# Optimization experiments

Hardware: AMD Instinct MI355X
Metric: run time of the kernel (lower is better)

Reference implementation:

```python
import jax, jax.numpy as jnp
import numpy as np

EMBED_DIMS = [8, 16, 8]      # prod = 1024 = embed_dim
HIDDEN_DIMS = [16, 16, 16]   # prod = 4096 = hidden_dim
RANK = 16
B, S = 4, 1024


def _make_cores(key, in_dims, out_dims, rank):
    d = len(in_dims)
    ranks = [1] + [rank] * (d - 1) + [1]
    cores = []
    for k in range(d):
        key, sub = jax.random.split(key)
        shape = (ranks[k], in_dims[k], out_dims[k], ranks[k + 1])
        scale = 1.0 / np.sqrt(in_dims[k] * ranks[k])
        cores.append((scale * jax.random.normal(sub, shape, dtype=jnp.float32)))
    return cores


def setup_inputs() -> dict:
    key = jax.random.key(0)
    k_x, k1, k2, kb1, kb2 = jax.random.split(key, 5)
    x = jax.random.normal(k_x, (B, S, 1024), dtype=jnp.float32)
    fc1 = _make_cores(k1, EMBED_DIMS, HIDDEN_DIMS, RANK)
    fc2 = _make_cores(k2, HIDDEN_DIMS, EMBED_DIMS, RANK)
    b1 = 0.01 * jax.random.normal(kb1, (4096,), dtype=jnp.float32)
    b2 = 0.01 * jax.random.normal(kb2, (1024,), dtype=jnp.float32)
    return {
        "x": x,
        "fc1_c0": fc1[0], "fc1_c1": fc1[1], "fc1_c2": fc1[2], "fc1_b": b1,
        "fc2_c0": fc2[0], "fc2_c1": fc2[1], "fc2_c2": fc2[2], "fc2_b": b2,
    }


def tt_linear(x_flat, cores, bias, in_dims):
    """TT-matrix x batch-of-vectors product. x_flat: [N, prod(in_dims)].

    Cores: core_k has shape [r_{k-1}, n_k, m_k, r_k] with r_0 = r_d = 1.
    Invariant: acc is [r_{k-1}, n_k, rest] with rest laid out as
    (n_{k+1}..n_d, N, m_1..m_{k-1}).
    """
    N = x_flat.shape[0]
    acc = x_flat.reshape((N,) + tuple(in_dims))      # [N, n1..nd]
    acc = jnp.moveaxis(acc, 0, -1)                   # [n1..nd, N]
    acc = acc.reshape(in_dims[0], -1)[None]          # [1, n1, rest]
    d = len(cores)
    for k, c in enumerate(cores):
        # contract previous rank + current input mode
        acc = jnp.einsum('pnR,pnmq->Rmq', acc, c)    # [rest, m_k, r_k]
        if k < d - 1:
            n_next = in_dims[k + 1]
            R, m, q = acc.shape
            acc = acc.reshape(n_next, R // n_next, m, q)
            acc = jnp.transpose(acc, (3, 0, 1, 2)).reshape(q, n_next, -1)
    # final acc: [N * m1..m_{d-1}, m_d, 1] -> [N, M]
    return acc.reshape(N, -1) + bias


def reference(x, fc1_c0, fc1_c1, fc1_c2, fc1_b, fc2_c0, fc2_c1, fc2_c2, fc2_b):
    flat = x.reshape(-1, x.shape[-1])                        # [N, embed_dim]
    z1 = tt_linear(flat, [fc1_c0, fc1_c1, fc1_c2], fc1_b, EMBED_DIMS)   # [N, hidden]
    h1 = jax.nn.gelu(z1, approximate=False)                  # exact erf GELU (torch default)
    z2 = tt_linear(h1, [fc2_c0, fc2_c1, fc2_c2], fc2_b, HIDDEN_DIMS)    # [N, embed]
    return z2.reshape(*x.shape[:-1], z2.shape[-1])
```

## Files before the change

### kernel.cpp

```cpp
#include <hip/hip_runtime.h>
#include <stdint.h>

__device__ __forceinline__ float b2f(unsigned short u) {
    union { uint32_t i; float f; } v; v.i = ((uint32_t)u) << 16; return v.f;
}
__device__ __forceinline__ unsigned short f2b(float f) {
    union { float f; uint32_t i; } v; v.f = f;
    uint32_t r = v.i + 0x7fffu + ((v.i >> 16) & 1u);
    return (unsigned short)(r >> 16);
}

typedef __bf16 bf16x8 __attribute__((ext_vector_type(8)));
typedef float  f32x16 __attribute__((ext_vector_type(16)));

__global__ __launch_bounds__(256)
void cvt_f32_bf16(const float* __restrict__ x, unsigned short* __restrict__ xb) {
    int t = blockIdx.x * 256 + threadIdx.x;
    const float4* p = (const float4*)(x + (size_t)t * 8);
    float4 f0 = p[0], f1 = p[1];
    int4 o;
    o.x = (uint32_t)f2b(f0.x) | ((uint32_t)f2b(f0.y) << 16);
    o.y = (uint32_t)f2b(f0.z) | ((uint32_t)f2b(f0.w) << 16);
    o.z = (uint32_t)f2b(f1.x) | ((uint32_t)f2b(f1.y) << 16);
    o.w = (uint32_t)f2b(f1.z) | ((uint32_t)f2b(f1.w) << 16);
    ((int4*)xb)[t] = o;
}

template<int N3, int M3>
__global__ void build_T(const float* __restrict__ c1,
                        const float* __restrict__ c2,
                        float* __restrict__ T) {
    int e = blockIdx.x * 256 + threadIdx.x;
    int m3 = e % M3;
    int t  = e / M3;
    int n3 = t % N3;
    int rm = t / N3;
    float s = 0.f;
#pragma unroll
    for (int r2 = 0; r2 < 16; ++r2)
        s += c1[rm * 16 + r2] * c2[(r2 * N3 + n3) * M3 + m3];
    T[e] = s;
}

template<int N1, int N2, int N3, int M1, int M2, int M3>
__global__ __launch_bounds__(256)
void build_W(const float* __restrict__ c0,
             const float* __restrict__ T,
             unsigned short* __restrict__ W) {
    constexpr int K = N1 * N2 * N3;
    int t  = blockIdx.x * 256 + threadIdx.x;
    int m3 = t % M3;
    int m2 = (t / M3) % M2;
    int n2 = (t / (M3 * M2)) % N2;
    int m1 = (t / (M3 * M2 * N2)) % M1;
    int n1 =  t / (M3 * M2 * N2 * M1);

    float c0r[16];
    const float4* c0p = (const float4*)(c0 + (n1 * M1 + m1) * 16);
#pragma unroll
    for (int i = 0; i < 4; ++i) ((float4*)c0r)[i] = c0p[i];

    float acc[N3] = {};
#pragma unroll
    for (int r1 = 0; r1 < 16; ++r1) {
        const float* Tp = T + (size_t)(((r1 * 16 + n2) * 16 + m2) * N3) * M3 + m3;
#pragma unroll
        for (int n3 = 0; n3 < N3; ++n3)
            acc[n3] += c0r[r1] * Tp[n3 * M3];
    }

    unsigned short ob[N3];
#pragma unroll
    for (int n3 = 0; n3 < N3; ++n3) ob[n3] = f2b(acc[n3]);

    unsigned short* dst = W + (size_t)((m1 * M2 + m2) * M3 + m3) * K
                            + (n1 * N2 + n2) * N3;
#pragma unroll
    for (int c = 0; c < N3 / 8; ++c)
        ((int4*)dst)[c] = ((const int4*)ob)[c];
}

template<int BM, int BN>
__device__ __forceinline__ void stage_chunk16(
    const unsigned short* __restrict__ A,
    const unsigned short* __restrict__ Bt,
    char* __restrict__ dstbuf, int ktot,
    int rowBase, int colBase, int tk, int c, int tid)
{
    const int off  = (c * 512 + tid) * 16;
    const bool isB = off >= BM * 128;
    const int off2 = isB ? off - BM * 128 : off;
    const int r    = off2 >> 7;
    const int jg   = ((off2 >> 4) & 7) ^ (r & 7);
    const unsigned short* src = (isB ? Bt + (size_t)(colBase + r) * ktot
                                     : A  + (size_t)(rowBase + r) * ktot)
                                + tk * 64 + jg * 8;
    void* dst = dstbuf + (c * 8192 + (tid >> 6) * 1024);
    __builtin_amdgcn_global_load_lds(
        (const __attribute__((address_space(1))) void*)src,
        (__attribute__((address_space(3))) void*)dst, 16, 0, 0);
}

template<int BM, int BN, int KTOT, int NCOLS, int PPT, bool DO_GELU, bool C_F32>
__global__ __launch_bounds__(512, 2)
void gemm3p(const unsigned short* __restrict__ A,
            const unsigned short* __restrict__ Bt,
            const float* __restrict__ bias,
            void* __restrict__ Cv)
{
    constexpr int BK   = 64;
    constexpr int NT   = KTOT / BK;
    constexpr int BUFB = (BM + BN) * 128;
    constexpr int LPT  = (BM + BN) * BK * 2 / (512 * 16);
    constexpr int SPP  = LPT / PPT;
    constexpr int KPP  = 4 / PPT;
    constexpr int WGM  = 4, WGN = 2;
    constexpr int FI   = BM / (WGM * 32);
    constexpr int FJ   = BN / (WGN * 32);
    constexpr int GX   = NCOLS / BN;

    extern __shared__ char smem[];

    const int tid  = threadIdx.x;
    const int lane = tid & 63;
    const int wave = tid >> 6;
    const int m32  = lane & 31;
    const int kh   = lane >> 5;
    const int wm   = wave >> 1;
    const int wn   = wave & 1;

    int lin = blockIdx.y * GX + blockIdx.x;
    const int cpx = (int)(GX * gridDim.y) >> 3;
    lin = (lin & 7) * cpx + (lin >> 3);
    const int rowBase = (lin / GX) * BM;
    const int colBase = (lin % GX) * BN;

    f32x16 acc[FI][FJ] = {};

#pragma unroll
    for (int c = 0; c < LPT; ++c)
        stage_chunk16<BM, BN>(A, Bt, smem, KTOT, rowBase, colBase, 0, c, tid);
#pragma unroll
    for (int c = 0; c < LPT; ++c)
        stage_chunk16<BM, BN>(A, Bt, smem + BUFB, KTOT, rowBase, colBase, 1, c, tid);
    asm volatile("s_waitcnt vmcnt(%0)" :: "n"(LPT) : "memory");
    __builtin_amdgcn_s_barrier();
    asm volatile("" ::: "memory");

    int bt = 0;
    for (int t = 0; t < NT; ++t) {
        const int sb = bt >= 1 ? bt - 1 : 2;
        const char* Ab = smem + bt * BUFB;
        const char* Bb = Ab + BM * 128;
        char* Sb = smem + sb * BUFB;
        const bool doStage = (t + 2 < NT);

#pragma unroll
        for (int ph = 0; ph < PPT; ++ph) {
            bf16x8 af[FI][KPP], bfr[FJ][KPP];
#pragma unroll
            for (int i = 0; i < FI; ++i) {
                const int rr = wm * (BM / WGM) + i * 32 + m32;
#pragma unroll
                for (int u = 0; u < KPP; ++u) {
                    const int lc = (ph * KPP + u) * 2 + kh;
                    af[i][u] = *(const bf16x8*)(Ab + rr * 128 + ((lc ^ (rr & 7)) << 4));
                }
            }
#pragma unroll
            for (int j = 0; j < FJ; ++j) {
                const int rr = wn * (BN / WGN) + j * 32 + m32;
#pragma unroll
                for (int u = 0; u < KPP; ++u) {
                    const int lc = (ph * KPP + u) * 2 + kh;
                    bfr[j][u] = *(const bf16x8*)(Bb + rr * 128 + ((lc ^ (rr & 7)) << 4));
                }
            }
            if (doStage) {
#pragma unroll
                for (int c = 0; c < SPP; ++c)
                    stage_chunk16<BM, BN>(A, Bt, Sb, KTOT, rowBase, colBase,
                                          t + 2, ph * SPP + c, tid);
            }
            __builtin_amdgcn_s_barrier();
            asm volatile("s_waitcnt lgkmcnt(0)" ::: "memory");
            __builtin_amdgcn_s_setprio(1);
#pragma unroll
            for (int u = 0; u < KPP; ++u)
#pragma unroll
                for (int i = 0; i < FI; ++i)
#pragma unroll
                    for (int j = 0; j < FJ; ++j)
                        acc[i][j] = __builtin_amdgcn_mfma_f32_32x32x16_bf16(
                            af[i][u], bfr[j][u], acc[i][j], 0, 0, 0);
            __builtin_amdgcn_s_setprio(0);
            if (ph == PPT - 1) {
                if (t + 2 < NT) {
                    asm volatile("s_waitcnt vmcnt(%0)" :: "n"(LPT) : "memory");
                } else if (t + 1 < NT) {
                    asm volatile("s_waitcnt vmcnt(0)" ::: "memory");
                }
            }
            __builtin_amdgcn_s_barrier();
            asm volatile("" ::: "memory");
        }
        bt = bt < 2 ? bt + 1 : 0;
    }

    const int waveM = wm * (BM / WGM);
    const int waveN = wn * (BN / WGN);
#pragma unroll
    for (int i = 0; i < FI; ++i) {
#pragma unroll
        for (int j = 0; j < FJ; ++j) {
            const int col = colBase + waveN + j * 32 + m32;
            const float bv = bias[col];
#pragma unroll
            for (int reg = 0; reg < 16; ++reg) {
                const int row = rowBase + waveM + i * 32 +
                                (reg & 3) + 8 * (reg >> 2) + 4 * kh;
                float z = acc[i][j][reg] + bv;
                if (DO_GELU)
                    z = 0.5f * z * (1.f + erff(z * 0.70710678118654752f));
                const size_t off = (size_t)row * NCOLS + col;
                if (C_F32) ((float*)Cv)[off] = z;
                else       ((unsigned short*)Cv)[off] = f2b(z);
            }
        }
    }
}

#define PC_COMPUTE(BUF)                                                       \
    {                                                                         \
        _Pragma("unroll")                                                     \
        for (int ks = 0; ks < 4; ++ks) {                                      \
            bf16x8 a_f[FI], b_f[FJ];                                          \
            _Pragma("unroll")                                                 \
            for (int i = 0; i < FI; ++i) {                                    \
                const int key = (m32 & 7) ^                                   \
                    (((waveM >> 3) + 4 * i + (m32 >> 3)) & 7);                \
                const int slot = ((ks * 2 + khalf) ^ key) * 8;                \
                a_f[i] = *(const bf16x8*)&As[(BUF) * ASZ +                    \
                          (waveM + i * 32 + m32) * BK + slot];                \
            }                                                                 \
            _Pragma("unroll")                                                 \
            for (int j = 0; j < FJ; ++j) {                                    \
                const int key = (m32 & 7) ^                                   \
                    (((waveN >> 3) + 4 * j + (m32 >> 3)) & 7);                \
                const int slot = ((ks * 2 + khalf) ^ key) * 8;                \
                b_f[j] = *(const bf16x8*)&Bs[(BUF) * BSZ +                    \
                          (waveN + j * 32 + m32) * BK + slot];                \
            }                                                                 \
            _Pragma("unroll")                                                 \
            for (int i = 0; i < FI; ++i)                                      \
                _Pragma("unroll")                                             \
                for (int j = 0; j < FJ; ++j)                                  \
                    acc[i][j] = __builtin_amdgcn_mfma_f32_32x32x16_bf16(      \
                        a_f[i], b_f[j], acc[i][j], 0, 0, 0);                  \
        }                                                                     \
    }

template<int BM, int BN, int KTOT, bool DO_GELU, bool A_F32, bool C_F32>
__global__ __launch_bounds__(512, 4)
void gemm_pc(const void* __restrict__ Av,
             const unsigned short* __restrict__ Bt,
             const float* __restrict__ bias,
             void* __restrict__ Cv,
             int Ncols) {
    constexpr int BK  = 64;
    constexpr int CA  = BM / 8;
    constexpr int CB  = BN / 8;
    constexpr int PA  = CA / 4;
    constexpr int PB  = CB / 4;
    constexpr int FI  = BM / 64;
    constexpr int FJ  = BN / 64;
    constexpr int ASZ = BM * BK;
    constexpr int BSZ = BN * BK;
    __shared__ unsigned short As[2 * ASZ];
    __shared__ unsigned short Bs[2 * BSZ];

    const int tid  = threadIdx.x;
    const int lane = tid & 63;
    const int wave = tid >> 6;
    const int rowBase = blockIdx.y * BM;
    const int colBase = blockIdx.x * BN;

    const int lr    = lane >> 3;
    const int jj    = lane & 7;
    const int m32   = lane & 31;
    const int khalf = lane >> 5;

    if (wave >= 4) {
        const int pw = wave - 4;
#pragma unroll
        for (int it = 0; it < PA; ++it) {
            const int c  = pw * PA + it;
            const int jg = jj ^ lr ^ (c & 7);
            const size_t aoff = (size_t)(rowBase + c * 8 + lr) * KTOT + jg * 8;
            int4 v;
            if (A_F32) {
                const float* ga = (const float*)Av + aoff;
                float4 f0 = *(const float4*)ga;
                float4 f1 = *(const float4*)(ga + 4);
                v.x = (uint32_t)f2b(f0.x) | ((uint32_t)f2b(f0.y) << 16);
                v.y = (uint32_t)f2b(f0.z) | ((uint32_t)f2b(f0.w) << 16);
                v.z = (uint32_t)f2b(f1.x) | ((uint32_t)f2b(f1.y) << 16);
                v.w = (uint32_t)f2b(f1.z) | ((uint32_t)f2b(f1.w) << 16);
            } else {
                v = *(const int4*)((const unsigned short*)Av + aoff);
            }
            *(int4*)&As[c * 512 + lane * 8] = v;
        }
#pragma unroll
        for (int it = 0; it < PB; ++it) {
            const int c  = pw * PB + it;
            const int jg = jj ^ lr ^ (c & 7);
            *(int4*)&Bs[c * 512 + lane * 8] =
                *(const int4*)(Bt + (size_t)(colBase + c * 8 + lr) * KTOT + jg * 8);
        }
        __syncthreads();

        int buf = 1;
        for (int k0 = BK; k0 < KTOT; k0 += BK) {
            int4 aR[PA], bR[PB];
#pragma unroll
            for (int it = 0; it < PA; ++it) {
                const int c  = pw * PA + it;
                const int jg = jj ^ lr ^ (c & 7);
                const size_t aoff = (size_t)(rowBase + c * 8 + lr) * KTOT + k0 + jg * 8;
                if (A_F32) {
                    const float* ga = (const float*)Av + aoff;
                    float4 f0 = *(const float4*)ga;
                    float4 f1 = *(const float4*)(ga + 4);
                    int4 v;
                    v.x = (uint32_t)f2b(f0.x) | ((uint32_t)f2b(f0.y) << 16);
                    v.y = (uint32_t)f2b(f0.z) | ((uint32_t)f2b(f0.w) << 16);
                    v.z = (uint32_t)f2b(f1.x) | ((uint32_t)f2b(f1.y) << 16);
                    v.w = (uint32_t)f2b(f1.z) | ((uint32_t)f2b(f1.w) << 16);
                    aR[it] = v;
                } else {
                    aR[it] = *(const int4*)((const unsigned short*)Av + aoff);
                }
            }
#pragma unroll
            for (int it = 0; it < PB; ++it) {
                const int c  = pw * PB + it;
                const int jg = jj ^ lr ^ (c & 7);
                bR[it] = *(const int4*)(Bt + (size_t)(colBase + c * 8 + lr) * KTOT + k0 + jg * 8);
            }
#pragma unroll
            for (int it = 0; it < PA; ++it) {
                const int c = pw * PA + it;
                *(int4*)&As[buf * ASZ + c * 512 + lane * 8] = aR[it];
            }
#pragma unroll
            for (int it = 0; it < PB; ++it) {
                const int c = pw * PB + it;
                *(int4*)&Bs[buf * BSZ + c * 512 + lane * 8] = bR[it];
            }
            __syncthreads();
            buf ^= 1;
        }
    } else {
        const int waveM = (wave >> 1) * (BM / 2);
        const int waveN = (wave & 1) * (BN / 2);
        f32x16 acc[FI][FJ] = {};

        __syncthreads();

        int cur = 0;
        for (int k0 = BK; k0 < KTOT; k0 += BK) {
            PC_COMPUTE(cur)
            __syncthreads();
            cur ^= 1;
        }
        PC_COMPUTE(cur)

#pragma unroll
        for (int i = 0; i < FI; ++i) {
#pragma unroll
            for (int j = 0; j < FJ; ++j) {
                const int col = colBase + waveN + j * 32 + m32;
                const float bv = bias[col];
#pragma unroll
                for (int reg = 0; reg < 16; ++reg) {
                    const int row = rowBase + waveM + i * 32 +
                                    (reg & 3) + 8 * (reg >> 2) + 4 * khalf;
                    float z = acc[i][j][reg] + bv;
                    if (DO_GELU)
                        z = 0.5f * z * (1.f + erff(z * 0.70710678118654752f));
                    const size_t off = (size_t)row * Ncols + col;
                    if (C_F32) ((float*)Cv)[off] = z;
                    else       ((unsigned short*)Cv)[off] = f2b(z);
                }
            }
        }
    }
}

extern "C" void kernel_launch(void* const* d_in, const int* in_sizes, int n_in,
                              void* d_out, int out_size, void* d_ws, size_t ws_size,
                              hipStream_t stream) {
    const float* x      = (const float*)d_in[0];
    const float* fc1_c0 = (const float*)d_in[1];
    const float* fc1_c1 = (const float*)d_in[2];
    const float* fc1_c2 = (const float*)d_in[3];
    const float* fc1_b  = (const float*)d_in[4];
    const float* fc2_c0 = (const float*)d_in[5];
    const float* fc2_c1 = (const float*)d_in[6];
    const float* fc2_c2 = (const float*)d_in[7];
    const float* fc2_b  = (const float*)d_in[8];

    char* ws = (char*)d_ws;
    unsigned short* W  = (unsigned short*)(ws);
    float*          T  = (float*)(ws + (8u << 20));
    const bool big = ws_size >= (50ull << 20);
    unsigned short* xb = (unsigned short*)(ws + (10u << 20));
    unsigned short* h  = (unsigned short*)(ws + (big ? (18u << 20) : (10u << 20)));

    static bool attr_done = false;
    if (!attr_done) {
        attr_done = true;
        (void)hipFuncSetAttribute(
            reinterpret_cast<const void*>(&gemm3p<256, 128, 1024, 4096, 2, true, false>),
            hipFuncAttributeMaxDynamicSharedMemorySize, 3 * (256 + 128) * 128);
        (void)hipFuncSetAttribute(
            reinterpret_cast<const void*>(&gemm3p<128, 128, 4096, 1024, 1, false, true>),
            hipFuncAttributeMaxDynamicSharedMemorySize, 3 * (128 + 128) * 128);
    }

    build_T<8, 16><<<2048, 256, 0, stream>>>(fc1_c1, fc1_c2, T);
    build_W<8, 16, 8, 16, 16, 16><<<2048, 256, 0, stream>>>(fc1_c0, T, W);
    if (big) {
        cvt_f32_bf16<<<2048, 256, 0, stream>>>(x, xb);
        gemm3p<256, 128, 1024, 4096, 2, true, false>
            <<<dim3(32, 16), 512, 3 * (256 + 128) * 128, stream>>>(xb, W, fc1_b, h);
    } else {
        gemm_pc<128, 128, 1024, true, true, false>
            <<<dim3(32, 32), 512, 0, stream>>>(x, W, fc1_b, h, 4096);
    }

    build_T<16, 8><<<2048, 256, 0, stream>>>(fc2_c1, fc2_c2, T);
    build_W<16, 16, 16, 8, 16, 8><<<1024, 256, 0, stream>>>(fc2_c0, T, W);
    gemm3p<128, 128, 4096, 1024, 1, false, true>
        <<<dim3(8, 32), 512, 3 * (128 + 128) * 128, stream>>>(h, W, fc2_b, d_out);
}
```

Measured before the change: 237.5 us.

## Use 256x256 tiles with 4-stage BK=32 pipeline and split-K atomics for fc2

Replaces the GEMM kernel with a 256x256 tile variant that uses BK=32, a 4-deep LDS ring buffer and a new swizzle with precomputed per-fragment offsets. The second GEMM becomes split-K over 4 chunks: the output is pre-filled with bias and partial sums are accumulated with atomic float adds. This aims to raise arithmetic intensity per tile and fill more CUs in the fc2 GEMM, which previously had only 256 blocks. In exchange it adds atomic traffic, an extra bias-fill pass, and non-deterministic summation order.

Result: slower. 259.4 us (+9.2%).

```diff
diff --git a/kernel.cpp b/kernel.cpp
--- a/kernel.cpp
+++ b/kernel.cpp
@@ -24,6 +24,12 @@
     o.z = (uint32_t)f2b(f1.x) | ((uint32_t)f2b(f1.y) << 16);
     o.w = (uint32_t)f2b(f1.z) | ((uint32_t)f2b(f1.w) << 16);
     ((int4*)xb)[t] = o;
+}
+
+__global__ __launch_bounds__(256)
+void bias_fill(const float* __restrict__ b, float4* __restrict__ out) {
+    int t = blockIdx.x * 256 + threadIdx.x;
+    out[t] = ((const float4*)b)[t & 255];
 }
 
 template<int N3, int M3>
@@ -81,43 +87,44 @@
 }
 
 template<int BM, int BN>
-__device__ __forceinline__ void stage_chunk16(
-    const unsigned short* __restrict__ A,
-    const unsigned short* __restrict__ Bt,
-    char* __restrict__ dstbuf, int ktot,
-    int rowBase, int colBase, int tk, int c, int tid)
+__device__ __forceinline__ void stage4(const unsigned short* __restrict__ A,
+                                       const unsigned short* __restrict__ Bt,
+                                       char* __restrict__ dstbuf, int kstride,
+                                       int rowBase, int colBase, int kElem,
+                                       int c, int tid)
 {
     const int off  = (c * 512 + tid) * 16;
-    const bool isB = off >= BM * 128;
-    const int off2 = isB ? off - BM * 128 : off;
-    const int r    = off2 >> 7;
-    const int jg   = ((off2 >> 4) & 7) ^ (r & 7);
-    const unsigned short* src = (isB ? Bt + (size_t)(colBase + r) * ktot
-                                     : A  + (size_t)(rowBase + r) * ktot)
-                                + tk * 64 + jg * 8;
+    const bool isB = off >= BM * 64;
+    const int off2 = isB ? off - BM * 64 : off;
+    const int r    = off2 >> 6;
+    const int slot = (off2 >> 4) & 3;
+    const int key  = ((r >> 1) ^ (r >> 3)) & 3;
+    const int g    = slot ^ key;
+    const unsigned short* src = (isB ? Bt + (size_t)(colBase + r) * kstride
+                                     : A  + (size_t)(rowBase + r) * kstride)
+                                + kElem + g * 8;
     void* dst = dstbuf + (c * 8192 + (tid >> 6) * 1024);
     __builtin_amdgcn_global_load_lds(
         (const __attribute__((address_space(1))) void*)src,
         (__attribute__((address_space(3))) void*)dst, 16, 0, 0);
 }
 
-template<int BM, int BN, int KTOT, int NCOLS, int PPT, bool DO_GELU, bool C_F32>
+template<int BM, int BN, int KCH, int NCOLS, int GX, int GY,
+         bool DO_GELU, bool ATOMIC>
 __global__ __launch_bounds__(512, 2)
-void gemm3p(const unsigned short* __restrict__ A,
+void gemm4r(const unsigned short* __restrict__ A,
             const unsigned short* __restrict__ Bt,
             const float* __restrict__ bias,
-            void* __restrict__ Cv)
+            void* __restrict__ Cv,
+            int kstride)
 {
-    constexpr int BK   = 64;
-    constexpr int NT   = KTOT / BK;
-    constexpr int BUFB = (BM + BN) * 128;
+    constexpr int BK   = 32;
+    constexpr int NT   = KCH / BK;
+    constexpr int BUFB = (BM + BN) * 64;
     constexpr int LPT  = (BM + BN) * BK * 2 / (512 * 16);
-    constexpr int SPP  = LPT / PPT;
-    constexpr int KPP  = 4 / PPT;
-    constexpr int WGM  = 4, WGN = 2;
-    constexpr int FI   = BM / (WGM * 32);
-    constexpr int FJ   = BN / (WGN * 32);
-    constexpr int GX   = NCOLS / BN;
+    constexpr int WGM = 2, WGN = 4;
+    constexpr int FI = BM / (WGM * 32);
+    constexpr int FJ = BN / (WGN * 32);
 
     extern __shared__ char smem[];
 
@@ -126,85 +133,89 @@
     const int wave = tid >> 6;
     const int m32  = lane & 31;
     const int kh   = lane >> 5;
-    const int wm   = wave >> 1;
-    const int wn   = wave & 1;
-
-    int lin = blockIdx.y * GX + blockIdx.x;
-    const int cpx = (int)(GX * gridDim.y) >> 3;
+    const int wm   = wave >> 2;
+    const int wn   = wave & 3;
+
+    int lin = ((int)blockIdx.z * GY + (int)blockIdx.y) * GX + (int)blockIdx.x;
+    const int total = GX * GY * (int)gridDim.z;
+    const int cpx = total >> 3;
     lin = (lin & 7) * cpx + (lin >> 3);
-    const int rowBase = (lin / GX) * BM;
-    const int colBase = (lin % GX) * BN;
+    const int colT = lin % GX;
+    const int rowT = (lin / GX) % GY;
+    const int kz   = lin / (GX * GY);
+    const int rowBase = rowT * BM;
+    const int colBase = colT * BN;
+    const int kOff    = kz * KCH;
+
+    int aOff[FI], aKey[FI];
+#pragma unroll
+    for (int i = 0; i < FI; ++i) {
+        const int r = wm * (BM / WGM) + i * 32 + m32;
+        aOff[i] = r * 64;
+        aKey[i] = ((r >> 1) ^ (r >> 3)) & 3;
+    }
+    int bOff[FJ], bKey[FJ];
+#pragma unroll
+    for (int j = 0; j < FJ; ++j) {
+        const int r = wn * (BN / WGN) + j * 32 + m32;
+        bOff[j] = BM * 64 + r * 64;
+        bKey[j] = ((r >> 1) ^ (r >> 3)) & 3;
+    }
 
     f32x16 acc[FI][FJ] = {};
 
 #pragma unroll
-    for (int c = 0; c < LPT; ++c)
-        stage_chunk16<BM, BN>(A, Bt, smem, KTOT, rowBase, colBase, 0, c, tid);
-#pragma unroll
-    for (int c = 0; c < LPT; ++c)
-        stage_chunk16<BM, BN>(A, Bt, smem + BUFB, KTOT, rowBase, colBase, 1, c, tid);
-    asm volatile("s_waitcnt vmcnt(%0)" :: "n"(LPT) : "memory");
+    for (int tt = 0; tt < 3; ++tt)
+#pragma unroll
+        for (int c = 0; c < LPT; ++c)
+            stage4<BM, BN>(A, Bt, smem + tt * BUFB, kstride,
+                           rowBase, colBase, kOff + tt * BK, c, tid);
+    asm volatile("s_waitcnt vmcnt(8)" ::: "memory");
     __builtin_amdgcn_s_barrier();
     asm volatile("" ::: "memory");
 
-    int bt = 0;
     for (int t = 0; t < NT; ++t) {
-        const int sb = bt >= 1 ? bt - 1 : 2;
-        const char* Ab = smem + bt * BUFB;
-        const char* Bb = Ab + BM * 128;
-        char* Sb = smem + sb * BUFB;
-        const bool doStage = (t + 2 < NT);
-
-#pragma unroll
-        for (int ph = 0; ph < PPT; ++ph) {
-            bf16x8 af[FI][KPP], bfr[FJ][KPP];
-#pragma unroll
-            for (int i = 0; i < FI; ++i) {
-                const int rr = wm * (BM / WGM) + i * 32 + m32;
-#pragma unroll
-                for (int u = 0; u < KPP; ++u) {
-                    const int lc = (ph * KPP + u) * 2 + kh;
-                    af[i][u] = *(const bf16x8*)(Ab + rr * 128 + ((lc ^ (rr & 7)) << 4));
-                }
-            }
-#pragma unroll
-            for (int j = 0; j < FJ; ++j) {
-                const int rr = wn * (BN / WGN) + j * 32 + m32;
-#pragma unroll
-                for (int u = 0; u < KPP; ++u) {
-                    const int lc = (ph * KPP + u) * 2 + kh;
-                    bfr[j][u] = *(const bf16x8*)(Bb + rr * 128 + ((lc ^ (rr & 7)) << 4));
-                }
-            }
-            if (doStage) {
-#pragma unroll
-                for (int c = 0; c < SPP; ++c)
-                    stage_chunk16<BM, BN>(A, Bt, Sb, KTOT, rowBase, colBase,
-                                          t + 2, ph * SPP + c, tid);
-            }
-            __builtin_amdgcn_s_barrier();
-            asm volatile("s_waitcnt lgkmcnt(0)" ::: "memory");
-            __builtin_amdgcn_s_setprio(1);
-#pragma unroll
-            for (int u = 0; u < KPP; ++u)
-#pragma unroll
-                for (int i = 0; i < FI; ++i)
-#pragma unroll
-                    for (int j = 0; j < FJ; ++j)
-                        acc[i][j] = __builtin_amdgcn_mfma_f32_32x32x16_bf16(
-                            af[i][u], bfr[j][u], acc[i][j], 0, 0, 0);
-            __builtin_amdgcn_s_setprio(0);
-            if (ph == PPT - 1) {
-                if (t + 2 < NT) {
-                    asm volatile("s_waitcnt vmcnt(%0)" :: "n"(LPT) : "memory");
-                } else if (t + 1 < NT) {
-                    asm volatile("s_waitcnt vmcnt(0)" ::: "memory");
-                }
-            }
+        char* base = smem + (t & 3) * BUFB;
+
+        if (t + 3 < NT) {
+            char* sb = smem + ((t + 3) & 3) * BUFB;
+#pragma unroll
+            for (int c = 0; c < LPT; ++c)
+                stage4<BM, BN>(A, Bt, sb, kstride, rowBase, colBase,
+                               kOff + (t + 3) * BK, c, tid);
+        }
+
+        __builtin_amdgcn_s_setprio(1);
+#pragma unroll
+        for (int u = 0; u < 2; ++u) {
+            bf16x8 af[FI], bfr[FJ];
+            const int lc = u * 2 + kh;
+#pragma unroll
+            for (int i = 0; i < FI; ++i)
+                af[i] = *(const bf16x8*)(base + aOff[i] + ((lc ^ aKey[i]) << 4));
+#pragma unroll
+            for (int j = 0; j < FJ; ++j)
+                bfr[j] = *(const bf16x8*)(base + bOff[j] + ((lc ^ bKey[j]) << 4));
+#pragma unroll
+            for (int i = 0; i < FI; ++i)
+#pragma unroll
+                for (int j = 0; j < FJ; ++j)
+                    acc[i][j] = __builtin_amdgcn_mfma_f32_32x32x16_bf16(
+                        af[i], bfr[j], acc[i][j], 0, 0, 0);
+        }
+        __builtin_amdgcn_s_setprio(0);
+
+        if (t + 3 < NT) {
+            asm volatile("s_waitcnt vmcnt(8)" ::: "memory");
+        } else if (t + 2 < NT) {
+            asm volatile("s_waitcnt vmcnt(4)" ::: "memory");
+        } else if (t + 1 < NT) {
+            asm volatile("s_waitcnt vmcnt(0)" ::: "memory");
+        }
+        if (t + 1 < NT) {
             __builtin_amdgcn_s_barrier();
             asm volatile("" ::: "memory");
         }
-        bt = bt < 2 ? bt + 1 : 0;
     }
 
     const int waveM = wm * (BM / WGM);
@@ -214,17 +225,20 @@
 #pragma unroll
         for (int j = 0; j < FJ; ++j) {
             const int col = colBase + waveN + j * 32 + m32;
-            const float bv = bias[col];
+            const float bv = ATOMIC ? 0.f : bias[col];
 #pragma unroll
             for (int reg = 0; reg < 16; ++reg) {
                 const int row = rowBase + waveM + i * 32 +
                                 (reg & 3) + 8 * (reg >> 2) + 4 * kh;
-                float z = acc[i][j][reg] + bv;
-                if (DO_GELU)
-                    z = 0.5f * z * (1.f + erff(z * 0.70710678118654752f));
                 const size_t off = (size_t)row * NCOLS + col;
-                if (C_F32) ((float*)Cv)[off] = z;
-                else       ((unsigned short*)Cv)[off] = f2b(z);
+                if (ATOMIC) {
+                    unsafeAtomicAdd((float*)Cv + off, acc[i][j][reg]);
+                } else {
+                    float z = acc[i][j][reg] + bv;
+                    if (DO_GELU)
+                        z = 0.5f * z * (1.f + erff(z * 0.70710678118654752f));
+                    ((unsigned short*)Cv)[off] = f2b(z);
+                }
             }
         }
     }
@@ -418,23 +432,27 @@
     unsigned short* xb = (unsigned short*)(ws + (10u << 20));
     unsigned short* h  = (unsigned short*)(ws + (big ? (18u << 20) : (10u << 20)));
 
+    constexpr int DLDS = 4 * (256 + 256) * 64;
+
     static bool attr_done = false;
     if (!attr_done) {
         attr_done = true;
         (void)hipFuncSetAttribute(
-            reinterpret_cast<const void*>(&gemm3p<256, 128, 1024, 4096, 2, true, false>),
-            hipFuncAttributeMaxDynamicSharedMemorySize, 3 * (256 + 128) * 128);
+            reinterpret_cast<const void*>(
+                &gemm4r<256, 256, 1024, 4096, 16, 16, true, false>),
+            hipFuncAttributeMaxDynamicSharedMemorySize, DLDS);
         (void)hipFuncSetAttribute(
-            reinterpret_cast<const void*>(&gemm3p<128, 128, 4096, 1024, 1, false, true>),
-            hipFuncAttributeMaxDynamicSharedMemorySize, 3 * (128 + 128) * 128);
+            reinterpret_cast<const void*>(
+                &gemm4r<256, 256, 1024, 1024, 4, 16, false, true>),
+            hipFuncAttributeMaxDynamicSharedMemorySize, DLDS);
     }
 
     build_T<8, 16><<<2048, 256, 0, stream>>>(fc1_c1, fc1_c2, T);
     build_W<8, 16, 8, 16, 16, 16><<<2048, 256, 0, stream>>>(fc1_c0, T, W);
     if (big) {
         cvt_f32_bf16<<<2048, 256, 0, stream>>>(x, xb);
-        gemm3p<256, 128, 1024, 4096, 2, true, false>
-            <<<dim3(32, 16), 512, 3 * (256 + 128) * 128, stream>>>(xb, W, fc1_b, h);
+        gemm4r<256, 256, 1024, 4096, 16, 16, true, false>
+            <<<dim3(16, 16, 1), 512, DLDS, stream>>>(xb, W, fc1_b, h, 1024);
     } else {
         gemm_pc<128, 128, 1024, true, true, false>
             <<<dim3(32, 32), 512, 0, stream>>>(x, W, fc1_b, h, 4096);
@@ -442,6 +460,12 @@
 
     build_T<16, 8><<<2048, 256, 0, stream>>>(fc2_c1, fc2_c2, T);
     build_W<16, 16, 16, 8, 16, 8><<<1024, 256, 0, stream>>>(fc2_c0, T, W);
-    gemm3p<128, 128, 4096, 1024, 1, false, true>
-        <<<dim3(8, 32), 512, 3 * (128 + 128) * 128, stream>>>(h, W, fc2_b, d_out);
-}
+    if (big) {
+        bias_fill<<<4096, 256, 0, stream>>>(fc2_b, (float4*)d_out);
+        gemm4r<256, 256, 1024, 1024, 4, 16, false, true>
+            <<<dim3(4, 16, 4), 512, DLDS, stream>>>(h, W, fc2_b, d_out, 4096);
+    } else {
+        gemm_pc<128, 64, 4096, false, false, true>
+            <<<dim3(16, 32), 512, 0, stream>>>(h, W, fc2_b, d_out, 1024);
+    }
+}
```
